# Optimization experiments

Hardware: AMD Instinct MI355X
Metric: run time of the kernel (lower is better)

The kernel has to match this reference:

```python
import jax, jax.numpy as jnp
import numpy as np

INPUT_SIZE = 32
HIDDEN_SIZE = 128
N_HEAD = 8
NER_NUMS = 8
D = INPUT_SIZE * NER_NUMS  # 256, attention feature dim per head


def setup_inputs() -> dict:
    key = jax.random.key(0)
    ks = jax.random.split(key, 10)
    B, S = 8, 2048
    x = jax.random.normal(ks[0], (B, S, D), dtype=jnp.float32)
    bi_lstm_o = jax.random.normal(ks[1], (B, S, 2 * HIDDEN_SIZE), dtype=jnp.float32)
    # per-head linear params, stacked on leading head axis (nn.init.normal_ -> std 1)
    Qw = jax.random.normal(ks[2], (N_HEAD, 2 * HIDDEN_SIZE, D), dtype=jnp.float32)
    Qb = jax.random.normal(ks[3], (N_HEAD, D), dtype=jnp.float32)
    Kw = jax.random.normal(ks[4], (N_HEAD, D, D), dtype=jnp.float32)
    Kb = jax.random.normal(ks[5], (N_HEAD, D), dtype=jnp.float32)
    Vw = jax.random.normal(ks[6], (N_HEAD, D, D), dtype=jnp.float32)
    Vb = jax.random.normal(ks[7], (N_HEAD, D), dtype=jnp.float32)
    Cw = jax.random.normal(ks[8], (N_HEAD * D, NER_NUMS), dtype=jnp.float32)
    Cb = jax.random.normal(ks[9], (NER_NUMS,), dtype=jnp.float32)
    return {"x": x, "bi_lstm_o": bi_lstm_o, "Qw": Qw, "Qb": Qb, "Kw": Kw,
            "Kb": Kb, "Vw": Vw, "Vb": Vb, "Cw": Cw, "Cb": Cb}


def reference(x, bi_lstm_o, Qw, Qb, Kw, Kb, Vw, Vb, Cw, Cb):
    # q from bi_lstm_o, k/v from x; all heads batched on axis h
    q = jnp.einsum('bsf,hfd->hbsd', bi_lstm_o, Qw) + Qb[:, None, None, :]
    k = jnp.einsum('bsf,hfd->hbsd', x, Kw) + Kb[:, None, None, :]
    v = jnp.einsum('bsf,hfd->hbsd', x, Vw) + Vb[:, None, None, :]
    scale = 1.0 / jnp.sqrt(jnp.float32(D))
    scores = jnp.einsum('hbsd,hbtd->hbst', q, k) * scale  # [H,B,S,S]
    attn = jax.nn.softmax(scores, axis=-1)
    o = jnp.einsum('hbst,hbtd->hbsd', attn, v)  # [H,B,S,D]
    B, S = x.shape[0], x.shape[1]
    concat = jnp.transpose(o, (1, 2, 0, 3)).reshape(B, S, N_HEAD * D)  # head order matches torch.cat
    return concat @ Cw + Cb
```

## Files before the change

kernel.cpp:

```cpp
#include <hip/hip_runtime.h>

#define H_ 8
#define B_ 8
#define S_ 2048
#define D_ 256

#define KSTRIDE 264
#define VSTRIDE 40
#define QTSTRIDE 136

typedef __attribute__((ext_vector_type(8))) _Float16 half8;
typedef __attribute__((ext_vector_type(4))) _Float16 half4v;
typedef __attribute__((ext_vector_type(2))) _Float16 half2v;
typedef __attribute__((ext_vector_type(4))) float f32x4;

__device__ inline void split8(const float* __restrict__ p, half8& hv, half8& lv) {
  float4 a = *(const float4*)p, b = *(const float4*)(p + 4);
  hv[0] = (_Float16)a.x; hv[1] = (_Float16)a.y; hv[2] = (_Float16)a.z; hv[3] = (_Float16)a.w;
  hv[4] = (_Float16)b.x; hv[5] = (_Float16)b.y; hv[6] = (_Float16)b.z; hv[7] = (_Float16)b.w;
  lv[0] = (_Float16)(a.x - (float)hv[0]); lv[1] = (_Float16)(a.y - (float)hv[1]);
  lv[2] = (_Float16)(a.z - (float)hv[2]); lv[3] = (_Float16)(a.w - (float)hv[3]);
  lv[4] = (_Float16)(b.x - (float)hv[4]); lv[5] = (_Float16)(b.y - (float)hv[5]);
  lv[6] = (_Float16)(b.z - (float)hv[6]); lv[7] = (_Float16)(b.w - (float)hv[7]);
}

__global__ void split_w_kernel(const float* __restrict__ W,
                               _Float16* __restrict__ thi, _Float16* __restrict__ tlo) {
  __shared__ float t[64][65];
  const int h = blockIdx.z, f0 = blockIdx.x * 64, d0 = blockIdx.y * 64;
  const int col = threadIdx.x & 63, rg = threadIdx.x >> 6;
#pragma unroll
  for (int it = 0; it < 16; ++it) {
    int f = rg * 16 + it;
    t[f][col] = W[((size_t)h * 256 + f0 + f) * 256 + d0 + col];
  }
  __syncthreads();
#pragma unroll
  for (int it = 0; it < 16; ++it) {
    int d = rg * 16 + it;
    float v = t[col][d];
    _Float16 hv = (_Float16)v;
    size_t idx = ((size_t)h * 256 + d0 + d) * 256 + f0 + col;
    thi[idx] = hv;
    tlo[idx] = (_Float16)(v - (float)hv);
  }
}

__global__ void out_init_kernel(float* __restrict__ out, const float* __restrict__ Cb) {
  int i = blockIdx.x * blockDim.x + threadIdx.x;
  if (i < B_ * S_ * 8) out[i] = Cb[i & 7];
}

template <int VMODE>
__global__ __launch_bounds__(256, 2) void proj_kernel(
    const float* __restrict__ A,
    const _Float16* __restrict__ Whi, const _Float16* __restrict__ Wlo,
    const float* __restrict__ bias, float oscale, int h0,
    _Float16* __restrict__ Ohi, _Float16* __restrict__ Olo) {
  constexpr bool TMULT = (VMODE != 1);
  __shared__ _Float16 a_hi[128 * VSTRIDE] __attribute__((aligned(16)));
  __shared__ _Float16 b_hi[128 * VSTRIDE] __attribute__((aligned(16)));
  __shared__ _Float16 a_lo[TMULT ? 128 * VSTRIDE : 8] __attribute__((aligned(16)));
  __shared__ _Float16 b_lo[TMULT ? 128 * VSTRIDE : 8] __attribute__((aligned(16)));
  const int tid = threadIdx.x;
  const int w = tid >> 6, lane = tid & 63;
  const int quad = lane >> 4, l15 = lane & 15;
  const int hb = blockIdx.z, h = h0 + (hb >> 3), b = hb & 7;
  const int s0 = blockIdx.x * 128, d0 = blockIdx.y * 128;
  const int wr = w >> 1, wc = w & 1;
  const f32x4 fz = {0.f, 0.f, 0.f, 0.f};
  f32x4 acc[4][4];
#pragma unroll
  for (int i = 0; i < 4; ++i)
#pragma unroll
    for (int j = 0; j < 4; ++j) acc[i][j] = fz;
  const size_t arow0 = (size_t)b * S_ + s0;
  const size_t wrow0 = (size_t)h * 256 + d0;
  for (int kk = 0; kk < 8; ++kk) {
    const int f0 = kk * 32;
    __syncthreads();
#pragma unroll
    for (int i = 0; i < 2; ++i) {
      int cc = i * 256 + tid;
      int r = cc >> 2, ch = (cc & 3) * 8;
      half8 hv, lv;
      split8(A + (arow0 + r) * 256 + f0 + ch, hv, lv);
      *(half8*)&a_hi[r * VSTRIDE + ch] = hv;
      size_t woff = (wrow0 + r) * 256 + f0 + ch;
      *(half8*)&b_hi[r * VSTRIDE + ch] = *(const half8*)(Whi + woff);
      if (TMULT) {
        *(half8*)&a_lo[r * VSTRIDE + ch] = lv;
        *(half8*)&b_lo[r * VSTRIDE + ch] = *(const half8*)(Wlo + woff);
      }
    }
    __syncthreads();
    half8 afh[4], afl[4], bfh[4], bfl[4];
#pragma unroll
    for (int t = 0; t < 4; ++t) {
      int ar = wr * 64 + t * 16 + l15;
      afh[t] = *(const half8*)&a_hi[ar * VSTRIDE + quad * 8];
      int br = wc * 64 + t * 16 + l15;
      bfh[t] = *(const half8*)&b_hi[br * VSTRIDE + quad * 8];
      if (TMULT) {
        afl[t] = *(const half8*)&a_lo[ar * VSTRIDE + quad * 8];
        bfl[t] = *(const half8*)&b_lo[br * VSTRIDE + quad * 8];
      }
    }
#pragma unroll
    for (int rf = 0; rf < 4; ++rf)
#pragma unroll
      for (int cf = 0; cf < 4; ++cf) {
        acc[rf][cf] = __builtin_amdgcn_mfma_f32_16x16x32_f16(afh[rf], bfh[cf], acc[rf][cf], 0, 0, 0);
        if (TMULT) {
          acc[rf][cf] = __builtin_amdgcn_mfma_f32_16x16x32_f16(afh[rf], bfl[cf], acc[rf][cf], 0, 0, 0);
          acc[rf][cf] = __builtin_amdgcn_mfma_f32_16x16x32_f16(afl[rf], bfh[cf], acc[rf][cf], 0, 0, 0);
        }
      }
  }
#pragma unroll
  for (int rf = 0; rf < 4; ++rf) {
#pragma unroll
    for (int cf = 0; cf < 4; ++cf) {
      const int d = d0 + wc * 64 + cf * 16 + l15;
      const float bv = bias[h * 256 + d];
      if (VMODE != 1) {
#pragma unroll
        for (int r = 0; r < 4; ++r) {
          const int s = s0 + wr * 64 + rf * 16 + quad * 4 + r;
          float val = (acc[rf][cf][r] + bv) * oscale;
          _Float16 hvv = (_Float16)val;
          size_t idx = ((size_t)hb * S_ + s) * 256 + d;
          Ohi[idx] = hvv;
          if (VMODE == 0) Olo[idx] = (_Float16)(val - (float)hvv);
        }
      } else {
        half4v pack;
#pragma unroll
        for (int r = 0; r < 4; ++r) pack[r] = (_Float16)((acc[rf][cf][r] + bv) * oscale);
        size_t idx = ((size_t)hb * 256 + d) * S_ + s0 + wr * 64 + rf * 16 + quad * 4;
        *(half4v*)(Ohi + idx) = pack;
      }
    }
  }
}

__device__ inline unsigned int pack2(float a, float b) {
  half2v h; h[0] = (_Float16)a; h[1] = (_Float16)b;
  return __builtin_bit_cast(unsigned int, h);
}

__global__ __launch_bounds__(256, 2) void flash_kernel(
    const float* __restrict__ bo,
    const _Float16* __restrict__ qwhi, const _Float16* __restrict__ qwlo,
    const float* __restrict__ qbias,
    const _Float16* __restrict__ khi,
    const _Float16* __restrict__ vt, const float* __restrict__ Cw,
    float* __restrict__ out, int h0) {
  __shared__ _Float16 smem[37376] __attribute__((aligned(16)));
  _Float16* qw_hi = smem + 8448;
  _Float16* qw_lo = smem + 27136;
  _Float16* bo_hi = smem;
  _Float16* bo_lo = smem + 2560;
  _Float16* qtb   = smem + 8448;
  const int tid = threadIdx.x, w = tid >> 6, lane = tid & 63;
  const int quad = lane >> 4, l15 = lane & 15;
  const int hb = blockIdx.y, h = h0 + (hb >> 3), b = hb & 7;
  const int qbase = blockIdx.x * 64;

  const f32x4 fz = {0.f, 0.f, 0.f, 0.f};
  f32x4 qacc[16];
#pragma unroll
  for (int df = 0; df < 16; ++df) qacc[df] = fz;
  for (int kk = 0; kk < 8; ++kk) {
    __syncthreads();
#pragma unroll
    for (int i = 0; i < 4; ++i) {
      int c = i * 256 + tid;
      int dr = c >> 2, ch = (c & 3) * 8;
      size_t woff = ((size_t)h * 256 + dr) * 256 + kk * 32 + ch;
      *(half8*)&qw_hi[dr * VSTRIDE + ch] = *(const half8*)(qwhi + woff);
      *(half8*)&qw_lo[dr * VSTRIDE + ch] = *(const half8*)(qwlo + woff);
    }
    {
      int rrow = tid >> 2, ch = (tid & 3) * 8;
      half8 hv, lv;
      split8(bo + ((size_t)b * S_ + qbase + rrow) * 256 + kk * 32 + ch, hv, lv);
      *(half8*)&bo_hi[rrow * VSTRIDE + ch] = hv;
      *(half8*)&bo_lo[rrow * VSTRIDE + ch] = lv;
    }
    __syncthreads();
    half8 bh = *(const half8*)&bo_hi[(w * 16 + l15) * VSTRIDE + quad * 8];
    half8 bl = *(const half8*)&bo_lo[(w * 16 + l15) * VSTRIDE + quad * 8];
#pragma unroll
    for (int df = 0; df < 16; ++df) {
      half8 awh = *(const half8*)&qw_hi[(df * 16 + l15) * VSTRIDE + quad * 8];
      half8 awl = *(const half8*)&qw_lo[(df * 16 + l15) * VSTRIDE + quad * 8];
      qacc[df] = __builtin_amdgcn_mfma_f32_16x16x32_f16(awh, bh, qacc[df], 0, 0, 0);
      qacc[df] = __builtin_amdgcn_mfma_f32_16x16x32_f16(awl, bh, qacc[df], 0, 0, 0);
      qacc[df] = __builtin_amdgcn_mfma_f32_16x16x32_f16(awh, bl, qacc[df], 0, 0, 0);
    }
  }

  half8 stK[4], stV[4];
  auto LOADKV = [&](int kt) {
    size_t kbase = ((size_t)hb * S_ + (size_t)kt * 32) * 256;
#pragma unroll
    for (int i = 0; i < 4; ++i) {
      int cc = i * 256 + tid;
      int kr = cc >> 5, kch = (cc & 31) * 8;
      stK[i] = *(const half8*)(khi + kbase + kr * 256 + kch);
      int vd = cc >> 2, vch = (cc & 3) * 8;
      stV[i] = *(const half8*)(vt + ((size_t)hb * 256 + vd) * S_ + (size_t)kt * 32 + vch);
    }
  };
  LOADKV(0);

  half8 qfh[8], qfl[8];
#pragma unroll
  for (int ph = 0; ph < 4; ++ph) {
    const int dh = ph >> 1;
    const bool lo = ph & 1;
    __syncthreads();
#pragma unroll
    for (int dfi = 0; dfi < 8; ++dfi) {
      int df = dh * 8 + dfi;
#pragma unroll
      for (int rp = 0; rp < 2; ++rp) {
        half2v hw;
#pragma unroll
        for (int rr2 = 0; rr2 < 2; ++rr2) {
          int r = rp * 2 + rr2;
          float bv = qbias[h * 256 + df * 16 + quad * 4 + r];
          float val = (qacc[df][r] + bv) * 0.0625f;
          _Float16 hv = (_Float16)val;
          hw[rr2] = lo ? (_Float16)(val - (float)hv) : hv;
        }
        *(half2v*)&qtb[(w * 16 + l15) * QTSTRIDE + dfi * 16 + quad * 4 + rp * 2] = hw;
      }
    }
    __syncthreads();
#pragma unroll
    for (int k2 = 0; k2 < 4; ++k2) {
      half8 v = *(const half8*)&qtb[(w * 16 + l15) * QTSTRIDE + k2 * 32 + quad * 8];
      if (lo) qfl[dh * 4 + k2] = v;
      else    qfh[dh * 4 + k2] = v;
    }
  }
  __syncthreads();

#pragma unroll
  for (int i = 0; i < 4; ++i) {
    int cc = i * 256 + tid;
    int kr = cc >> 5, kch = (cc & 31) * 8;
    *(half8*)&smem[kr * KSTRIDE + kch] = stK[i];
    int vd = cc >> 2, vch = (cc & 3) * 8;
    *(half8*)&smem[8448 + vd * VSTRIDE + vch] = stV[i];
  }
  LOADKV(1);
  __syncthreads();

  f32x4 o_acc[16];
#pragma unroll
  for (int df = 0; df < 16; ++df) o_acc[df] = fz;
  float m_r = -3.0e38f, l_r = 0.f;

  for (int kt = 0; kt < 64; ++kt) {
    _Float16* kbuf = smem + (kt & 1) * 18688;
    _Float16* vbuf = kbuf + 8448;
    if (kt < 63) {
      _Float16* kw = smem + ((kt + 1) & 1) * 18688;
      _Float16* vw = kw + 8448;
#pragma unroll
      for (int i = 0; i < 4; ++i) {
        int cc = i * 256 + tid;
        int kr = cc >> 5, kch = (cc & 31) * 8;
        *(half8*)&kw[kr * KSTRIDE + kch] = stK[i];
        int vd = cc >> 2, vch = (cc & 3) * 8;
        *(half8*)&vw[vd * VSTRIDE + vch] = stV[i];
      }
      if (kt < 62) LOADKV(kt + 2);
    }
    f32x4 sc0 = fz, sc1 = fz;
#pragma unroll
    for (int ks = 0; ks < 8; ++ks) {
      half8 bh0 = *(const half8*)&kbuf[(0 * 16 + l15) * KSTRIDE + ks * 32 + quad * 8];
      sc0 = __builtin_amdgcn_mfma_f32_16x16x32_f16(bh0, qfh[ks], sc0, 0, 0, 0);
      sc0 = __builtin_amdgcn_mfma_f32_16x16x32_f16(bh0, qfl[ks], sc0, 0, 0, 0);
      half8 bh1 = *(const half8*)&kbuf[(1 * 16 + l15) * KSTRIDE + ks * 32 + quad * 8];
      sc1 = __builtin_amdgcn_mfma_f32_16x16x32_f16(bh1, qfh[ks], sc1, 0, 0, 0);
      sc1 = __builtin_amdgcn_mfma_f32_16x16x32_f16(bh1, qfl[ks], sc1, 0, 0, 0);
    }
    float v = fmaxf(fmaxf(fmaxf(sc0[0], sc0[1]), fmaxf(sc0[2], sc0[3])),
                    fmaxf(fmaxf(sc1[0], sc1[1]), fmaxf(sc1[2], sc1[3])));
    v = fmaxf(v, __shfl_xor(v, 16));
    v = fmaxf(v, __shfl_xor(v, 32));
    if (__any(v > m_r + 8.0f)) {
      const float mn = fmaxf(m_r, v);
      const float al = __expf(m_r - mn);
      m_r = mn;
      l_r *= al;
      float al_r[4];
#pragma unroll
      for (int r = 0; r < 4; ++r) al_r[r] = __shfl(al, quad * 4 + r);
#pragma unroll
      for (int df = 0; df < 16; ++df)
#pragma unroll
        for (int r = 0; r < 4; ++r) o_acc[df][r] *= al_r[r];
    }
    float p0[4], p1[4], s = 0.f;
#pragma unroll
    for (int r = 0; r < 4; ++r) {
      p0[r] = __expf(sc0[r] - m_r);
      p1[r] = __expf(sc1[r] - m_r);
      s += p0[r] + p1[r];
    }
    s += __shfl_xor(s, 16);
    s += __shfl_xor(s, 32);
    l_r += s;
    {
      unsigned int u0 = pack2(p0[0], p0[1]), u1 = pack2(p0[2], p0[3]);
      unsigned int v0 = pack2(p1[0], p1[1]), v1 = pack2(p1[2], p1[3]);
      const int src0 = ((quad & 1) << 5) + l15;
      const int src1 = src0 + 16;
      unsigned int a0 = __shfl(u0, src0), a1 = __shfl(u1, src0);
      unsigned int a2 = __shfl(u0, src1), a3 = __shfl(u1, src1);
      unsigned int c0 = __shfl(v0, src0), c1 = __shfl(v1, src0);
      unsigned int c2 = __shfl(v0, src1), c3 = __shfl(v1, src1);
      union U { unsigned int u[4]; half8 h; } pu;
      const bool hiq = quad >= 2;
      pu.u[0] = hiq ? c0 : a0;
      pu.u[1] = hiq ? c1 : a1;
      pu.u[2] = hiq ? c2 : a2;
      pu.u[3] = hiq ? c3 : a3;
      half8 pf = pu.h;
#pragma unroll
      for (int df = 0; df < 16; ++df) {
        half8 vf = *(const half8*)&vbuf[(df * 16 + l15) * VSTRIDE + quad * 8];
        o_acc[df] = __builtin_amdgcn_mfma_f32_16x16x32_f16(pf, vf, o_acc[df], 0, 0, 0);
      }
    }
    __syncthreads();
  }
  float rcl[4];
#pragma unroll
  for (int r = 0; r < 4; ++r) rcl[r] = 1.0f / __shfl(l_r, quad * 4 + r);
  float part[32];
#pragma unroll
  for (int i = 0; i < 32; ++i) part[i] = 0.f;
#pragma unroll
  for (int df = 0; df < 16; ++df) {
    const float4* cwv = (const float4*)(Cw + ((size_t)h * 256 + df * 16 + l15) * 8);
    float4 c0 = cwv[0], c1 = cwv[1];
#pragma unroll
    for (int r = 0; r < 4; ++r) {
      float ov = o_acc[df][r] * rcl[r];
      part[r * 8 + 0] += ov * c0.x;
      part[r * 8 + 1] += ov * c0.y;
      part[r * 8 + 2] += ov * c0.z;
      part[r * 8 + 3] += ov * c0.w;
      part[r * 8 + 4] += ov * c1.x;
      part[r * 8 + 5] += ov * c1.y;
      part[r * 8 + 6] += ov * c1.z;
      part[r * 8 + 7] += ov * c1.w;
    }
  }
#pragma unroll
  for (int i = 0; i < 32; ++i) {
    float v = part[i];
    v += __shfl_xor(v, 1);
    v += __shfl_xor(v, 2);
    v += __shfl_xor(v, 4);
    v += __shfl_xor(v, 8);
    part[i] = v;
  }
  if (l15 == 0) {
#pragma unroll
    for (int r = 0; r < 4; ++r) {
      int s = qbase + w * 16 + quad * 4 + r;
#pragma unroll
      for (int j = 0; j < 8; ++j)
        atomicAdd(&out[((size_t)b * S_ + s) * 8 + j], part[r * 8 + j]);
    }
  }
}

extern "C" void kernel_launch(void* const* d_in, const int* in_sizes, int n_in,
                              void* d_out, int out_size, void* d_ws, size_t ws_size,
                              hipStream_t stream) {
  const float* x  = (const float*)d_in[0];
  const float* bo = (const float*)d_in[1];
  const float* Qw = (const float*)d_in[2];
  const float* Qb = (const float*)d_in[3];
  const float* Kw = (const float*)d_in[4];
  const float* Kb = (const float*)d_in[5];
  const float* Vw = (const float*)d_in[6];
  const float* Vb = (const float*)d_in[7];
  const float* Cw = (const float*)d_in[8];
  const float* Cb = (const float*)d_in[9];
  float* out = (float*)d_out;

  const size_t NW  = (size_t)H_ * 256 * 256;
  const size_t NHB = (size_t)B_ * S_ * 256;
  const size_t ALN = 256;
  auto pad = [](size_t b) { return (b + 255) & ~(size_t)255; };

  int HC = 8;
  while (HC > 1) {
    size_t need = 6 * pad(NW * 2) + 2 * pad((size_t)HC * NHB * 2) + ALN;
    if (need <= ws_size) break;
    HC >>= 1;
  }

  char* base = (char*)d_ws;
  size_t off = 0;
  auto carve = [&](size_t nelem) -> _Float16* {
    _Float16* p = (_Float16*)(base + off);
    off += pad(nelem * 2);
    return p;
  };
  _Float16* qwt_hi = carve(NW); _Float16* qwt_lo = carve(NW);
  _Float16* kwt_hi = carve(NW); _Float16* kwt_lo = carve(NW);
  _Float16* vwt_hi = carve(NW); _Float16* vwt_lo = carve(NW);
  const size_t NC = (size_t)HC * NHB;
  _Float16* k_hi = carve(NC);
  _Float16* v_t  = carve(NC);

  dim3 wg(4, 4, 8);
  split_w_kernel<<<wg, 256, 0, stream>>>(Qw, qwt_hi, qwt_lo);
  split_w_kernel<<<wg, 256, 0, stream>>>(Kw, kwt_hi, kwt_lo);
  split_w_kernel<<<wg, 256, 0, stream>>>(Vw, vwt_hi, vwt_lo);
  out_init_kernel<<<(B_ * S_ * 8) / 256, 256, 0, stream>>>(out, Cb);

  for (int h0 = 0; h0 < H_; h0 += HC) {
    dim3 pg(16, 2, HC * 8);
    proj_kernel<2><<<pg, 256, 0, stream>>>(x, kwt_hi, kwt_lo, Kb, 1.0f, h0, k_hi, nullptr);
    proj_kernel<1><<<pg, 256, 0, stream>>>(x, vwt_hi, vwt_lo, Vb, 1.0f, h0, v_t, nullptr);
    dim3 fg(32, HC * 8);
    flash_kernel<<<fg, 256, 0, stream>>>(bo, qwt_hi, qwt_lo, Qb, k_hi, v_t, Cw, out, h0);
  }
}
```

Measured before the change: 807.3 us.

## Process two 64-row query groups per flash block to reuse K/V tiles

Each flash block now handles 128 query rows as two 64-row groups, so every K/V tile staged in shared memory feeds twice as many MFMAs. This halves the grid and the global/LDS traffic for K and V per query row. In exchange, register use roughly doubles (two sets of accumulators and Q fragments), occupancy drops to one block per SIMD set via launch bounds, and the smaller grid may leave CUs underfilled. The bo_lo staging offset is moved so the 128-row tile fits.

After: 943.5 us. +16.9%, slower.

```diff
diff --git a/kernel.cpp b/kernel.cpp
--- a/kernel.cpp
+++ b/kernel.cpp
@@ -149,7 +149,7 @@
   return __builtin_bit_cast(unsigned int, h);
 }
 
-__global__ __launch_bounds__(256, 2) void flash_kernel(
+__global__ __launch_bounds__(256, 1) void flash_kernel(
     const float* __restrict__ bo,
     const _Float16* __restrict__ qwhi, const _Float16* __restrict__ qwlo,
     const float* __restrict__ qbias,
@@ -160,17 +160,19 @@
   _Float16* qw_hi = smem + 8448;
   _Float16* qw_lo = smem + 27136;
   _Float16* bo_hi = smem;
-  _Float16* bo_lo = smem + 2560;
+  _Float16* bo_lo = smem + 18688;
   _Float16* qtb   = smem + 8448;
   const int tid = threadIdx.x, w = tid >> 6, lane = tid & 63;
   const int quad = lane >> 4, l15 = lane & 15;
   const int hb = blockIdx.y, h = h0 + (hb >> 3), b = hb & 7;
-  const int qbase = blockIdx.x * 64;
+  const int qbase = blockIdx.x * 128;
 
   const f32x4 fz = {0.f, 0.f, 0.f, 0.f};
-  f32x4 qacc[16];
-#pragma unroll
-  for (int df = 0; df < 16; ++df) qacc[df] = fz;
+  f32x4 qacc[2][16];
+#pragma unroll
+  for (int g = 0; g < 2; ++g)
+#pragma unroll
+    for (int df = 0; df < 16; ++df) qacc[g][df] = fz;
   for (int kk = 0; kk < 8; ++kk) {
     __syncthreads();
 #pragma unroll
@@ -181,23 +183,28 @@
       *(half8*)&qw_hi[dr * VSTRIDE + ch] = *(const half8*)(qwhi + woff);
       *(half8*)&qw_lo[dr * VSTRIDE + ch] = *(const half8*)(qwlo + woff);
     }
-    {
-      int rrow = tid >> 2, ch = (tid & 3) * 8;
+#pragma unroll
+    for (int j = 0; j < 2; ++j) {
+      int cc = j * 256 + tid;
+      int rrow = cc >> 2, ch = (cc & 3) * 8;
       half8 hv, lv;
       split8(bo + ((size_t)b * S_ + qbase + rrow) * 256 + kk * 32 + ch, hv, lv);
       *(half8*)&bo_hi[rrow * VSTRIDE + ch] = hv;
       *(half8*)&bo_lo[rrow * VSTRIDE + ch] = lv;
     }
     __syncthreads();
-    half8 bh = *(const half8*)&bo_hi[(w * 16 + l15) * VSTRIDE + quad * 8];
-    half8 bl = *(const half8*)&bo_lo[(w * 16 + l15) * VSTRIDE + quad * 8];
-#pragma unroll
-    for (int df = 0; df < 16; ++df) {
-      half8 awh = *(const half8*)&qw_hi[(df * 16 + l15) * VSTRIDE + quad * 8];
-      half8 awl = *(const half8*)&qw_lo[(df * 16 + l15) * VSTRIDE + quad * 8];
-      qacc[df] = __builtin_amdgcn_mfma_f32_16x16x32_f16(awh, bh, qacc[df], 0, 0, 0);
-      qacc[df] = __builtin_amdgcn_mfma_f32_16x16x32_f16(awl, bh, qacc[df], 0, 0, 0);
-      qacc[df] = __builtin_amdgcn_mfma_f32_16x16x32_f16(awh, bl, qacc[df], 0, 0, 0);
+#pragma unroll
+    for (int g = 0; g < 2; ++g) {
+      half8 bh = *(const half8*)&bo_hi[(g * 64 + w * 16 + l15) * VSTRIDE + quad * 8];
+      half8 bl = *(const half8*)&bo_lo[(g * 64 + w * 16 + l15) * VSTRIDE + quad * 8];
+#pragma unroll
+      for (int df = 0; df < 16; ++df) {
+        half8 awh = *(const half8*)&qw_hi[(df * 16 + l15) * VSTRIDE + quad * 8];
+        half8 awl = *(const half8*)&qw_lo[(df * 16 + l15) * VSTRIDE + quad * 8];
+        qacc[g][df] = __builtin_amdgcn_mfma_f32_16x16x32_f16(awh, bh, qacc[g][df], 0, 0, 0);
+        qacc[g][df] = __builtin_amdgcn_mfma_f32_16x16x32_f16(awl, bh, qacc[g][df], 0, 0, 0);
+        qacc[g][df] = __builtin_amdgcn_mfma_f32_16x16x32_f16(awh, bl, qacc[g][df], 0, 0, 0);
+      }
     }
   }
 
@@ -215,35 +222,38 @@
   };
   LOADKV(0);
 
-  half8 qfh[8], qfl[8];
-#pragma unroll
-  for (int ph = 0; ph < 4; ++ph) {
-    const int dh = ph >> 1;
-    const bool lo = ph & 1;
-    __syncthreads();
-#pragma unroll
-    for (int dfi = 0; dfi < 8; ++dfi) {
-      int df = dh * 8 + dfi;
-#pragma unroll
-      for (int rp = 0; rp < 2; ++rp) {
-        half2v hw;
-#pragma unroll
-        for (int rr2 = 0; rr2 < 2; ++rr2) {
-          int r = rp * 2 + rr2;
-          float bv = qbias[h * 256 + df * 16 + quad * 4 + r];
-          float val = (qacc[df][r] + bv) * 0.0625f;
-          _Float16 hv = (_Float16)val;
-          hw[rr2] = lo ? (_Float16)(val - (float)hv) : hv;
+  half8 qfh[2][8], qfl[2][8];
+#pragma unroll
+  for (int g = 0; g < 2; ++g) {
+#pragma unroll
+    for (int ph = 0; ph < 4; ++ph) {
+      const int dh = ph >> 1;
+      const bool lo = ph & 1;
+      __syncthreads();
+#pragma unroll
+      for (int dfi = 0; dfi < 8; ++dfi) {
+        int df = dh * 8 + dfi;
+#pragma unroll
+        for (int rp = 0; rp < 2; ++rp) {
+          half2v hw;
+#pragma unroll
+          for (int rr2 = 0; rr2 < 2; ++rr2) {
+            int r = rp * 2 + rr2;
+            float bv = qbias[h * 256 + df * 16 + quad * 4 + r];
+            float val = (qacc[g][df][r] + bv) * 0.0625f;
+            _Float16 hv = (_Float16)val;
+            hw[rr2] = lo ? (_Float16)(val - (float)hv) : hv;
+          }
+          *(half2v*)&qtb[(w * 16 + l15) * QTSTRIDE + dfi * 16 + quad * 4 + rp * 2] = hw;
         }
-        *(half2v*)&qtb[(w * 16 + l15) * QTSTRIDE + dfi * 16 + quad * 4 + rp * 2] = hw;
-      }
-    }
-    __syncthreads();
-#pragma unroll
-    for (int k2 = 0; k2 < 4; ++k2) {
-      half8 v = *(const half8*)&qtb[(w * 16 + l15) * QTSTRIDE + k2 * 32 + quad * 8];
-      if (lo) qfl[dh * 4 + k2] = v;
-      else    qfh[dh * 4 + k2] = v;
+      }
+      __syncthreads();
+#pragma unroll
+      for (int k2 = 0; k2 < 4; ++k2) {
+        half8 v = *(const half8*)&qtb[(w * 16 + l15) * QTSTRIDE + k2 * 32 + quad * 8];
+        if (lo) qfl[g][dh * 4 + k2] = v;
+        else    qfh[g][dh * 4 + k2] = v;
+      }
     }
   }
   __syncthreads();
@@ -259,10 +269,12 @@
   LOADKV(1);
   __syncthreads();
 
-  f32x4 o_acc[16];
-#pragma unroll
-  for (int df = 0; df < 16; ++df) o_acc[df] = fz;
-  float m_r = -3.0e38f, l_r = 0.f;
+  f32x4 o_acc[2][16];
+#pragma unroll
+  for (int g = 0; g < 2; ++g)
+#pragma unroll
+    for (int df = 0; df < 16; ++df) o_acc[g][df] = fz;
+  float m_r[2] = {-3.0e38f, -3.0e38f}, l_r[2] = {0.f, 0.f};
 
   for (int kt = 0; kt < 64; ++kt) {
     _Float16* kbuf = smem + (kt & 1) * 18688;
@@ -280,44 +292,49 @@
       }
       if (kt < 62) LOADKV(kt + 2);
     }
-    f32x4 sc0 = fz, sc1 = fz;
+    f32x4 sc0[2] = {fz, fz}, sc1[2] = {fz, fz};
 #pragma unroll
     for (int ks = 0; ks < 8; ++ks) {
       half8 bh0 = *(const half8*)&kbuf[(0 * 16 + l15) * KSTRIDE + ks * 32 + quad * 8];
-      sc0 = __builtin_amdgcn_mfma_f32_16x16x32_f16(bh0, qfh[ks], sc0, 0, 0, 0);
-      sc0 = __builtin_amdgcn_mfma_f32_16x16x32_f16(bh0, qfl[ks], sc0, 0, 0, 0);
       half8 bh1 = *(const half8*)&kbuf[(1 * 16 + l15) * KSTRIDE + ks * 32 + quad * 8];
-      sc1 = __builtin_amdgcn_mfma_f32_16x16x32_f16(bh1, qfh[ks], sc1, 0, 0, 0);
-      sc1 = __builtin_amdgcn_mfma_f32_16x16x32_f16(bh1, qfl[ks], sc1, 0, 0, 0);
-    }
-    float v = fmaxf(fmaxf(fmaxf(sc0[0], sc0[1]), fmaxf(sc0[2], sc0[3])),
-                    fmaxf(fmaxf(sc1[0], sc1[1]), fmaxf(sc1[2], sc1[3])));
-    v = fmaxf(v, __shfl_xor(v, 16));
-    v = fmaxf(v, __shfl_xor(v, 32));
-    if (__any(v > m_r + 8.0f)) {
-      const float mn = fmaxf(m_r, v);
-      const float al = __expf(m_r - mn);
-      m_r = mn;
-      l_r *= al;
-      float al_r[4];
-#pragma unroll
-      for (int r = 0; r < 4; ++r) al_r[r] = __shfl(al, quad * 4 + r);
-#pragma unroll
-      for (int df = 0; df < 16; ++df)
-#pragma unroll
-        for (int r = 0; r < 4; ++r) o_acc[df][r] *= al_r[r];
-    }
-    float p0[4], p1[4], s = 0.f;
-#pragma unroll
-    for (int r = 0; r < 4; ++r) {
-      p0[r] = __expf(sc0[r] - m_r);
-      p1[r] = __expf(sc1[r] - m_r);
-      s += p0[r] + p1[r];
-    }
-    s += __shfl_xor(s, 16);
-    s += __shfl_xor(s, 32);
-    l_r += s;
-    {
+#pragma unroll
+      for (int g = 0; g < 2; ++g) {
+        sc0[g] = __builtin_amdgcn_mfma_f32_16x16x32_f16(bh0, qfh[g][ks], sc0[g], 0, 0, 0);
+        sc0[g] = __builtin_amdgcn_mfma_f32_16x16x32_f16(bh0, qfl[g][ks], sc0[g], 0, 0, 0);
+        sc1[g] = __builtin_amdgcn_mfma_f32_16x16x32_f16(bh1, qfh[g][ks], sc1[g], 0, 0, 0);
+        sc1[g] = __builtin_amdgcn_mfma_f32_16x16x32_f16(bh1, qfl[g][ks], sc1[g], 0, 0, 0);
+      }
+    }
+    half8 pf[2];
+#pragma unroll
+    for (int g = 0; g < 2; ++g) {
+      float v = fmaxf(fmaxf(fmaxf(sc0[g][0], sc0[g][1]), fmaxf(sc0[g][2], sc0[g][3])),
+                      fmaxf(fmaxf(sc1[g][0], sc1[g][1]), fmaxf(sc1[g][2], sc1[g][3])));
+      v = fmaxf(v, __shfl_xor(v, 16));
+      v = fmaxf(v, __shfl_xor(v, 32));
+      if (__any(v > m_r[g] + 8.0f)) {
+        const float mn = fmaxf(m_r[g], v);
+        const float al = __expf(m_r[g] - mn);
+        m_r[g] = mn;
+        l_r[g] *= al;
+        float al_r[4];
+#pragma unroll
+        for (int r = 0; r < 4; ++r) al_r[r] = __shfl(al, quad * 4 + r);
+#pragma unroll
+        for (int df = 0; df < 16; ++df)
+#pragma unroll
+          for (int r = 0; r < 4; ++r) o_acc[g][df][r] *= al_r[r];
+      }
+      float p0[4], p1[4], s = 0.f;
+#pragma unroll
+      for (int r = 0; r < 4; ++r) {
+        p0[r] = __expf(sc0[g][r] - m_r[g]);
+        p1[r] = __expf(sc1[g][r] - m_r[g]);
+        s += p0[r] + p1[r];
+      }
+      s += __shfl_xor(s, 16);
+      s += __shfl_xor(s, 32);
+      l_r[g] += s;
       unsigned int u0 = pack2(p0[0], p0[1]), u1 = pack2(p0[2], p0[3]);
       unsigned int v0 = pack2(p1[0], p1[1]), v1 = pack2(p1[2], p1[3]);
       const int src0 = ((quad & 1) << 5) + l15;
@@ -332,54 +349,58 @@
       pu.u[1] = hiq ? c1 : a1;
       pu.u[2] = hiq ? c2 : a2;
       pu.u[3] = hiq ? c3 : a3;
-      half8 pf = pu.h;
-#pragma unroll
-      for (int df = 0; df < 16; ++df) {
-        half8 vf = *(const half8*)&vbuf[(df * 16 + l15) * VSTRIDE + quad * 8];
-        o_acc[df] = __builtin_amdgcn_mfma_f32_16x16x32_f16(pf, vf, o_acc[df], 0, 0, 0);
-      }
+      pf[g] = pu.h;
+    }
+#pragma unroll
+    for (int df = 0; df < 16; ++df) {
+      half8 vf = *(const half8*)&vbuf[(df * 16 + l15) * VSTRIDE + quad * 8];
+      o_acc[0][df] = __builtin_amdgcn_mfma_f32_16x16x32_f16(pf[0], vf, o_acc[0][df], 0, 0, 0);
+      o_acc[1][df] = __builtin_amdgcn_mfma_f32_16x16x32_f16(pf[1], vf, o_acc[1][df], 0, 0, 0);
     }
     __syncthreads();
   }
-  float rcl[4];
-#pragma unroll
-  for (int r = 0; r < 4; ++r) rcl[r] = 1.0f / __shfl(l_r, quad * 4 + r);
-  float part[32];
-#pragma unroll
-  for (int i = 0; i < 32; ++i) part[i] = 0.f;
-#pragma unroll
-  for (int df = 0; df < 16; ++df) {
-    const float4* cwv = (const float4*)(Cw + ((size_t)h * 256 + df * 16 + l15) * 8);
-    float4 c0 = cwv[0], c1 = cwv[1];
-#pragma unroll
-    for (int r = 0; r < 4; ++r) {
-      float ov = o_acc[df][r] * rcl[r];
-      part[r * 8 + 0] += ov * c0.x;
-      part[r * 8 + 1] += ov * c0.y;
-      part[r * 8 + 2] += ov * c0.z;
-      part[r * 8 + 3] += ov * c0.w;
-      part[r * 8 + 4] += ov * c1.x;
-      part[r * 8 + 5] += ov * c1.y;
-      part[r * 8 + 6] += ov * c1.z;
-      part[r * 8 + 7] += ov * c1.w;
-    }
-  }
-#pragma unroll
-  for (int i = 0; i < 32; ++i) {
-    float v = part[i];
-    v += __shfl_xor(v, 1);
-    v += __shfl_xor(v, 2);
-    v += __shfl_xor(v, 4);
-    v += __shfl_xor(v, 8);
-    part[i] = v;
-  }
-  if (l15 == 0) {
-#pragma unroll
-    for (int r = 0; r < 4; ++r) {
-      int s = qbase + w * 16 + quad * 4 + r;
-#pragma unroll
-      for (int j = 0; j < 8; ++j)
-        atomicAdd(&out[((size_t)b * S_ + s) * 8 + j], part[r * 8 + j]);
+#pragma unroll
+  for (int g = 0; g < 2; ++g) {
+    float rcl[4];
+#pragma unroll
+    for (int r = 0; r < 4; ++r) rcl[r] = 1.0f / __shfl(l_r[g], quad * 4 + r);
+    float part[32];
+#pragma unroll
+    for (int i = 0; i < 32; ++i) part[i] = 0.f;
+#pragma unroll
+    for (int df = 0; df < 16; ++df) {
+      const float4* cwv = (const float4*)(Cw + ((size_t)h * 256 + df * 16 + l15) * 8);
+      float4 c0 = cwv[0], c1 = cwv[1];
+#pragma unroll
+      for (int r = 0; r < 4; ++r) {
+        float ov = o_acc[g][df][r] * rcl[r];
+        part[r * 8 + 0] += ov * c0.x;
+        part[r * 8 + 1] += ov * c0.y;
+        part[r * 8 + 2] += ov * c0.z;
+        part[r * 8 + 3] += ov * c0.w;
+        part[r * 8 + 4] += ov * c1.x;
+        part[r * 8 + 5] += ov * c1.y;
+        part[r * 8 + 6] += ov * c1.z;
+        part[r * 8 + 7] += ov * c1.w;
+      }
+    }
+#pragma unroll
+    for (int i = 0; i < 32; ++i) {
+      float v = part[i];
+      v += __shfl_xor(v, 1);
+      v += __shfl_xor(v, 2);
+      v += __shfl_xor(v, 4);
+      v += __shfl_xor(v, 8);
+      part[i] = v;
+    }
+    if (l15 == 0) {
+#pragma unroll
+      for (int r = 0; r < 4; ++r) {
+        int s = qbase + g * 64 + w * 16 + quad * 4 + r;
+#pragma unroll
+        for (int j = 0; j < 8; ++j)
+          atomicAdd(&out[((size_t)b * S_ + s) * 8 + j], part[r * 8 + j]);
+      }
     }
   }
 }
@@ -435,7 +456,7 @@
     dim3 pg(16, 2, HC * 8);
     proj_kernel<2><<<pg, 256, 0, stream>>>(x, kwt_hi, kwt_lo, Kb, 1.0f, h0, k_hi, nullptr);
     proj_kernel<1><<<pg, 256, 0, stream>>>(x, vwt_hi, vwt_lo, Vb, 1.0f, h0, v_t, nullptr);
-    dim3 fg(32, HC * 8);
+    dim3 fg(16, HC * 8);
     flash_kernel<<<fg, 256, 0, stream>>>(bo, qwt_hi, qwt_lo, Qb, k_hi, v_t, Cw, out, h0);
   }
 }
```
